# Optimization experiments

Hardware: AMD Instinct MI355X
Metric: run time of the kernel (lower is better)

The kernel has to match this reference:

```python
import math
import jax, jax.numpy as jnp
import numpy as np

NUM_HEADS = 16
LN_EPS = 1e-5


def _ln(x, g, b):
    m = x.mean(-1, keepdims=True)
    v = ((x - m) ** 2).mean(-1, keepdims=True)
    return (x - m) * jax.lax.rsqrt(v + LN_EPS) * g + b


def _rotary_embedding(lat, lon, dim, base=10000.0):
    # spherical-geometry-aware rotary phases; returns sin/cos of shape lat.shape + [dim//2]
    pi = jnp.asarray(math.pi, lat.dtype)
    lon_wrapped = jnp.remainder(lon + pi, 2 * pi) - pi
    lat_c = jnp.clip(lat, -math.pi / 2 + 1e-6, math.pi / 2 - 1e-6)
    scaled_lon = lon_wrapped * jnp.cos(lat_c)
    half = dim // 2
    inv_freq = 1.0 / (base ** (jnp.arange(half, dtype=lat.dtype) / half))
    phase = (lat_c + scaled_lon)[..., None] * inv_freq
    return jnp.sin(phase), jnp.cos(phase)


def _apply_rotary(q, k, sin, cos):
    # q,k: [N, heads, S, hd]; sin/cos: [S, hd//2]
    sin = sin[None, None]
    cos = cos[None, None]
    def rot(x):
        x1 = x[..., 0::2]  # even lanes (torch view(...,hd//2,2).unbind(-1))
        x2 = x[..., 1::2]
        # torch concatenates the two rotated halves (no re-interleave)
        return jnp.concatenate([x1 * cos - x2 * sin, x1 * sin + x2 * cos], axis=-1)
    return rot(q), rot(k)


def _sdpa(q, k, v):
    scale = 1.0 / jnp.sqrt(jnp.asarray(q.shape[-1], q.dtype))
    s = jnp.einsum('nhqd,nhkd->nhqk', q, k) * scale
    return jnp.einsum('nhqk,nhkd->nhqd', jax.nn.softmax(s, axis=-1), v)


def _axial_block(tokens, g, bln, qkv_w, qkv_b, proj_w, proj_b, sincos):
    # tokens: [N, S, D] -> norm -> qkv -> (rope) -> sdpa -> proj -> residual
    N, S, D = tokens.shape
    hd = D // NUM_HEADS
    qkv = _ln(tokens, g, bln) @ qkv_w + qkv_b
    q, k, v = jnp.split(qkv, 3, axis=-1)
    def to_heads(t):
        return t.reshape(N, S, NUM_HEADS, hd).transpose(0, 2, 1, 3)
    q, k, v = to_heads(q), to_heads(k), to_heads(v)
    if sincos is not None:
        q, k = _apply_rotary(q, k, sincos[0], sincos[1])
    o = _sdpa(q, k, v).transpose(0, 2, 1, 3).reshape(N, S, D)
    return tokens + (o @ proj_w + proj_b)


def setup_inputs() -> dict:
    key = jax.random.key(0)
    ks = jax.random.split(key, 8)
    B, L, H, W, D = 1, 13, 48, 96, 512
    x = jax.random.normal(ks[0], (B, L, H, W, D), dtype=jnp.float32)
    lat_grid = jnp.linspace(-math.pi / 2 + 0.01, math.pi / 2 - 0.01, H, dtype=jnp.float32)
    lon_grid = jnp.linspace(-math.pi, math.pi, W, dtype=jnp.float32)  # unused by forward
    s = 0.02
    return {
        'x': x, 'lat_grid': lat_grid, 'lon_grid': lon_grid,
        'lat_qkv_w': s * jax.random.normal(ks[1], (D, 3 * D), jnp.float32),
        'lat_qkv_b': jnp.zeros((3 * D,), jnp.float32),
        'lon_qkv_w': s * jax.random.normal(ks[2], (D, 3 * D), jnp.float32),
        'lon_qkv_b': jnp.zeros((3 * D,), jnp.float32),
        'lev_qkv_w': s * jax.random.normal(ks[3], (D, 3 * D), jnp.float32),
        'lev_qkv_b': jnp.zeros((3 * D,), jnp.float32),
        'proj_w': s * jax.random.normal(ks[4], (D, D), jnp.float32),
        'proj_b': jnp.zeros((D,), jnp.float32),
        'g_lat': jnp.ones((D,), jnp.float32), 'b_lat': jnp.zeros((D,), jnp.float32),
        'g_lon': jnp.ones((D,), jnp.float32), 'b_lon': jnp.zeros((D,), jnp.float32),
        'g_lev': jnp.ones((D,), jnp.float32), 'b_lev': jnp.zeros((D,), jnp.float32),
    }


def reference(x, lat_grid, lon_grid, lat_qkv_w, lat_qkv_b, lon_qkv_w, lon_qkv_b,
              lev_qkv_w, lev_qkv_b, proj_w, proj_b,
              g_lat, b_lat, g_lon, b_lon, g_lev, b_lev):
    B, L, H, W, D = x.shape
    hd = D // NUM_HEADS
    # --- lat axis ---
    lat_tokens = x.transpose(0, 1, 3, 2, 4).reshape(B * L * W, H, D)
    lat_sin, lat_cos = _rotary_embedding(lat_grid, jnp.zeros_like(lat_grid), hd)
    lat_out = _axial_block(lat_tokens, g_lat, b_lat, lat_qkv_w, lat_qkv_b,
                           proj_w, proj_b, (lat_sin, lat_cos))
    lat_out = lat_out.reshape(B, L, W, H, D).transpose(0, 1, 3, 2, 4)
    # --- lon axis ---
    lon_tokens = lat_out.reshape(B * L * H, W, D)
    lon_range = jnp.linspace(-math.pi, math.pi, W, dtype=x.dtype)
    lon_sin, lon_cos = _rotary_embedding(jnp.zeros_like(lon_range), lon_range, hd)
    lon_out = _axial_block(lon_tokens, g_lon, b_lon, lon_qkv_w, lon_qkv_b,
                           proj_w, proj_b, (lon_sin, lon_cos))
    lon_out = lon_out.reshape(B, L, H, W, D)
    # --- level axis (no rotary) ---
    lev_tokens = lon_out.transpose(0, 2, 3, 1, 4).reshape(B * H * W, L, D)
    lev_out = _axial_block(lev_tokens, g_lev, b_lev, lev_qkv_w, lev_qkv_b,
                           proj_w, proj_b, None)
    return lev_out.reshape(B, H, W, L, D).transpose(0, 3, 1, 2, 4)
```

## Files before the change

### kernel.cpp

```cpp
#include <hip/hip_runtime.h>
#include <cstdint>


#define L_DIM 13
#define H_DIM 48
#define W_DIM 96
#define D_DIM 512
#define NH    16
#define MTOK  (L_DIM * H_DIM * W_DIM)
#define N3    (3 * D_DIM)
#define PI_F  3.14159265358979323846f

typedef __bf16 bf16x8 __attribute__((ext_vector_type(8)));
typedef float  f32x4  __attribute__((ext_vector_type(4)));

__device__ __forceinline__ float bf2f(unsigned short u) {
    return __builtin_bit_cast(float, ((unsigned)u) << 16);
}
__device__ __forceinline__ unsigned short f2bf(float f) {
    unsigned u = __builtin_bit_cast(unsigned, f);
    u += 0x7fffu + ((u >> 16) & 1u);
    return (unsigned short)(u >> 16);
}
__device__ __forceinline__ void gload16(unsigned short* lds, const unsigned short* g) {
    __builtin_amdgcn_global_load_lds(
        (const __attribute__((address_space(1))) unsigned int*)g,
        (__attribute__((address_space(3))) unsigned int*)lds, 16, 0, 0);
}

__global__ __launch_bounds__(256) void transpose_w(const float* __restrict__ w,
                                                   unsigned short* __restrict__ wt, int N) {
    __shared__ unsigned short t[64][65];
    const int k0 = blockIdx.x * 64, n0 = blockIdx.y * 64;
    const int tid = threadIdx.x;
    #pragma unroll
    for (int j = 0; j < 16; ++j) {
        int lin = j * 256 + tid;
        int kr = lin >> 6, nc = lin & 63;
        t[kr][nc] = f2bf(w[(size_t)(k0 + kr) * N + n0 + nc]);
    }
    __syncthreads();
    #pragma unroll
    for (int j = 0; j < 16; ++j) {
        int lin = j * 256 + tid;
        int nr = lin >> 6, kc = lin & 63;
        wt[(size_t)(n0 + nr) * 512 + k0 + kc] = t[kc][nr];
    }
}

__global__ __launch_bounds__(256) void ln_apply(
    const float* __restrict__ src, const float* __restrict__ g,
    const float* __restrict__ bln, unsigned short* __restrict__ out)
{
    int wv = threadIdx.x >> 6, lane = threadIdx.x & 63;
    int t = blockIdx.x * 4 + wv;
    const float* p = src + (size_t)t * 512 + lane * 8;
    float4 a = *(const float4*)p, b = *(const float4*)(p + 4);
    float s  = a.x + a.y + a.z + a.w + b.x + b.y + b.z + b.w;
    float s2 = a.x*a.x + a.y*a.y + a.z*a.z + a.w*a.w + b.x*b.x + b.y*b.y + b.z*b.z + b.w*b.w;
    #pragma unroll
    for (int off = 1; off < 64; off <<= 1) {
        s  += __shfl_xor(s, off, 64);
        s2 += __shfl_xor(s2, off, 64);
    }
    float mu = s * (1.f / 512.f);
    float rs = rsqrtf(s2 * (1.f / 512.f) - mu * mu + 1e-5f);
    float4 g0 = *(const float4*)(g + lane * 8),  g1 = *(const float4*)(g + lane * 8 + 4);
    float4 b0 = *(const float4*)(bln + lane * 8), b1 = *(const float4*)(bln + lane * 8 + 4);
    unsigned short o[8];
    o[0] = f2bf((a.x - mu) * rs * g0.x + b0.x);
    o[1] = f2bf((a.y - mu) * rs * g0.y + b0.y);
    o[2] = f2bf((a.z - mu) * rs * g0.z + b0.z);
    o[3] = f2bf((a.w - mu) * rs * g0.w + b0.w);
    o[4] = f2bf((b.x - mu) * rs * g1.x + b1.x);
    o[5] = f2bf((b.y - mu) * rs * g1.y + b1.y);
    o[6] = f2bf((b.z - mu) * rs * g1.z + b1.z);
    o[7] = f2bf((b.w - mu) * rs * g1.w + b1.w);
    uint4 r;
    r.x = (unsigned)o[0] | ((unsigned)o[1] << 16);
    r.y = (unsigned)o[2] | ((unsigned)o[3] << 16);
    r.z = (unsigned)o[4] | ((unsigned)o[5] << 16);
    r.w = (unsigned)o[6] | ((unsigned)o[7] << 16);
    *(uint4*)&out[(size_t)t * 512 + lane * 8] = r;
}

#define QUAD(mi, A) do { \
    acc[mi][0] = __builtin_amdgcn_mfma_f32_16x16x32_bf16(b0, A, acc[mi][0], 0, 0, 0); \
    acc[mi][1] = __builtin_amdgcn_mfma_f32_16x16x32_bf16(b1, A, acc[mi][1], 0, 0, 0); \
    acc[mi][2] = __builtin_amdgcn_mfma_f32_16x16x32_bf16(b2, A, acc[mi][2], 0, 0, 0); \
    acc[mi][3] = __builtin_amdgcn_mfma_f32_16x16x32_bf16(b3, A, acc[mi][3], 0, 0, 0); \
} while (0)
#define RDA(AS, mi, ks) (*(const bf16x8*)&AS[wm + (mi) * 16 + lm][((((ks) * 4 + kq) ^ (lm & 7)) << 3)])
#define RDB(BS, ni, ks) (*(const bf16x8*)&BS[wn + (ni) * 16 + lm][((((ks) * 4 + kq) ^ (lm & 7)) << 3)])

#define KTILE(CAs, CBs, NAs, NBs, kn, ST, LAST) do {                               \
    bf16x8 a0, a1, a2, a3, b0, b1, b2, b3;                                         \
                                              \
    a0 = RDA(CAs,0,0); a1 = RDA(CAs,1,0); a2 = RDA(CAs,2,0); a3 = RDA(CAs,3,0);    \
    b0 = RDB(CBs,0,0); b1 = RDB(CBs,1,0); b2 = RDB(CBs,2,0); b3 = RDB(CBs,3,0);    \
    if (ST) {                                                                      \
        gload16(&NBs[wv * 32 +  0][0], bsrc + (size_t) 0 * 512 + (kn));            \
        gload16(&NBs[wv * 32 +  8][0], bsrc + (size_t) 8 * 512 + (kn));            \
        gload16(&NBs[wv * 32 + 16][0], bsrc + (size_t)16 * 512 + (kn));            \
        gload16(&NBs[wv * 32 + 24][0], bsrc + (size_t)24 * 512 + (kn));            \
    }                                                                              \
    __builtin_amdgcn_s_barrier();                                                  \
    __builtin_amdgcn_s_setprio(1);                                                 \
    QUAD(0, a0); QUAD(1, a1); QUAD(2, a2); QUAD(3, a3);                            \
    __builtin_amdgcn_s_setprio(0);                                                 \
    if (ST) asm volatile("s_waitcnt vmcnt(4)" ::: "memory");    \
    else    asm volatile("s_waitcnt vmcnt(0)" ::: "memory");       \
    __builtin_amdgcn_s_barrier();                                                  \
    __builtin_amdgcn_sched_barrier(0);                                             \
                             \
    a0 = RDA(CAs,4,0); a1 = RDA(CAs,5,0); a2 = RDA(CAs,6,0); a3 = RDA(CAs,7,0);    \
    if (ST) {                                                                      \
        gload16(&NAs[ar0 + 0][0], asrc + (kn));                                    \
        gload16(&NAs[ar0 + 8][0], asrc + (size_t)8 * LDA + (kn));                  \
    }                                                                              \
    __builtin_amdgcn_s_barrier();                                                  \
    __builtin_amdgcn_s_setprio(1);                                                 \
    QUAD(4, a0); QUAD(5, a1); QUAD(6, a2); QUAD(7, a3);                            \
    __builtin_amdgcn_s_setprio(0);                                                 \
    __builtin_amdgcn_s_barrier();                                                  \
                                             \
    a0 = RDA(CAs,0,1); a1 = RDA(CAs,1,1); a2 = RDA(CAs,2,1); a3 = RDA(CAs,3,1);    \
    b0 = RDB(CBs,0,1); b1 = RDB(CBs,1,1); b2 = RDB(CBs,2,1); b3 = RDB(CBs,3,1);    \
    if (ST) {                                                                      \
        gload16(&NAs[ar0 + 64][0], asrc + (size_t)64 * LDA + (kn));                \
        gload16(&NAs[ar0 + 72][0], asrc + (size_t)72 * LDA + (kn));                \
    }                                                                              \
    __builtin_amdgcn_s_barrier();                                                  \
    __builtin_amdgcn_s_setprio(1);                                                 \
    QUAD(0, a0); QUAD(1, a1); QUAD(2, a2); QUAD(3, a3);                            \
    __builtin_amdgcn_s_setprio(0);                                                 \
    __builtin_amdgcn_s_barrier();                                                  \
                                                             \
    a0 = RDA(CAs,4,1); a1 = RDA(CAs,5,1); a2 = RDA(CAs,6,1); a3 = RDA(CAs,7,1);    \
    __builtin_amdgcn_s_barrier();                                                  \
    __builtin_amdgcn_s_setprio(1);                                                 \
    QUAD(4, a0); QUAD(5, a1); QUAD(6, a2); QUAD(7, a3);                            \
    __builtin_amdgcn_s_setprio(0);                                                 \
    if (ST) asm volatile("s_waitcnt vmcnt(2)" ::: "memory");   \
    if (!LAST) __builtin_amdgcn_s_barrier();                                       \
    __builtin_amdgcn_sched_barrier(0);                                             \
} while (0)

template<int LDA, int NBX, bool PROJ>
__global__ __launch_bounds__(512, 2) void gemm8p(
    const unsigned short* __restrict__ A,
    const unsigned short* __restrict__ B,
    const float* __restrict__ bias,
    const float* __restrict__ resid,
    float* __restrict__ outf,
    unsigned short* __restrict__ outh)
{
    __shared__ alignas(16) unsigned short As0[256][64];
    __shared__ alignas(16) unsigned short As1[256][64];
    __shared__ alignas(16) unsigned short Bs0[256][64];
    __shared__ alignas(16) unsigned short Bs1[256][64];

    const int nwg = NBX * 234;
    const int orig = blockIdx.y * NBX + blockIdx.x;
    const int qq = nwg >> 3, rr = nwg & 7;
    const int xcd = orig & 7, idx = orig >> 3;
    const int swz = (xcd < rr ? xcd * (qq + 1) : rr * (qq + 1) + (xcd - rr) * qq) + idx;
    const int n0 = (swz % NBX) * 256;
    const int m0 = (swz / NBX) * 256;

    const int tid = threadIdx.x, lane = tid & 63, wv = tid >> 6;
    const int wm = (wv >> 2) * 128, wn = (wv & 3) * 64;
    const int lm = lane & 15, kq = lane >> 4;
    const int rblk = lane >> 3;
    const int sc = (((lane & 7) ^ rblk) << 3);

    const unsigned short* bsrc = B + (size_t)(n0 + wv * 32 + rblk) * 512 + sc;
    const int ar0 = (wv & 4) ? (128 + (wv & 3) * 16) : (wv * 16);
    const unsigned short* asrc = A + (size_t)(m0 + ar0 + rblk) * LDA + sc;

    f32x4 acc[8][4] = {};

    #pragma unroll
    for (int j = 0; j < 4; ++j)
        gload16(&Bs0[wv * 32 + j * 8][0], bsrc + (size_t)(j * 8) * 512);
    gload16(&As0[ar0 + 0][0], asrc);
    gload16(&As0[ar0 + 8][0], asrc + (size_t)8 * LDA);
    gload16(&As0[ar0 + 64][0], asrc + (size_t)64 * LDA);
    gload16(&As0[ar0 + 72][0], asrc + (size_t)72 * LDA);
    asm volatile("s_waitcnt vmcnt(2)" ::: "memory");
    __builtin_amdgcn_s_barrier();
    __builtin_amdgcn_sched_barrier(0);

    for (int kt = 0; kt < 6; kt += 2) {
        KTILE(As0, Bs0, As1, Bs1, (kt + 1) * 64, true, false);
        KTILE(As1, Bs1, As0, Bs0, (kt + 2) * 64, true, false);
    }
    KTILE(As0, Bs0, As1, Bs1, 7 * 64, true, false);
    KTILE(As1, Bs1, As0, Bs0, 0, false, true);

    const int cr = kq << 2;
    if constexpr (!PROJ) {
        #pragma unroll
        for (int ni = 0; ni < 4; ++ni) {
            const int col = n0 + wn + ni * 16 + cr;
            const float4 bb = *(const float4*)&bias[col];
            #pragma unroll
            for (int mi = 0; mi < 8; ++mi) {
                const size_t off = (size_t)(m0 + wm + mi * 16 + lm) * N3 + col;
                uint2 pk;
                pk.x = (unsigned)f2bf(acc[mi][ni][0] + bb.x) | ((unsigned)f2bf(acc[mi][ni][1] + bb.y) << 16);
                pk.y = (unsigned)f2bf(acc[mi][ni][2] + bb.z) | ((unsigned)f2bf(acc[mi][ni][3] + bb.w) << 16);
                *(uint2*)&outh[off] = pk;
            }
        }
    } else {
        #pragma unroll
        for (int ni = 0; ni < 4; ++ni) {
            const int col = n0 + wn + ni * 16 + cr;
            const float4 bb = *(const float4*)&bias[col];
            #pragma unroll
            for (int mi = 0; mi < 8; ++mi) {
                const size_t off = (size_t)(m0 + wm + mi * 16 + lm) * 512 + col;
                float4 rs = *(const float4*)&resid[off];
                float4 o;
                o.x = rs.x + acc[mi][ni][0] + bb.x;
                o.y = rs.y + acc[mi][ni][1] + bb.y;
                o.z = rs.z + acc[mi][ni][2] + bb.z;
                o.w = rs.w + acc[mi][ni][3] + bb.w;
                *(float4*)&outf[off] = o;
            }
        }
    }
}

template<int S, int MODE>
__global__ __launch_bounds__(256) void attn_big(
    unsigned short* __restrict__ qkv,
    const float* __restrict__ lat_grid, const float* __restrict__ lon_grid)
{
    constexpr int NQ  = S / 16;
    constexpr int SKP = (S + 31) & ~31;
    constexpr int VST = SKP + 8;
    __shared__ alignas(16) unsigned short qs[S][40];
    __shared__ alignas(16) unsigned short ks[S][40];
    __shared__ alignas(16) unsigned short vT[32][VST];
    __shared__ alignas(16) unsigned short pb[4][16][VST];

    const int n = blockIdx.x, h = blockIdx.y;
    const int tid = threadIdx.x, lane = tid & 63, wv = tid >> 6;
    int base, step;
    if (MODE == 0) { int l = n / 96, w = n - l * 96; base = l * 4608 + w; step = 96; }
    else           { base = n * 96; step = 1; }

    const float SCALE = 0.17677669529663689f;
    for (int idx = tid; idx < S * 16; idx += 256) {
        int s = idx >> 4, i = idx & 15;
        size_t ro = (size_t)(base + s * step) * N3 + h * 32;
        unsigned qp = *(const unsigned*)(qkv + ro + 2 * i);
        unsigned kp = *(const unsigned*)(qkv + ro + 512 + 2 * i);
        unsigned vp = *(const unsigned*)(qkv + ro + 1024 + 2 * i);
        float coord;
        if (MODE == 0) {
            float la = lat_grid[s];
            coord = fminf(fmaxf(la, -PI_F / 2 + 1e-6f), PI_F / 2 - 1e-6f);
        } else {
            float xp = lon_grid[s] + PI_F;
            coord = xp - floorf(xp * (0.5f / PI_F)) * (2.f * PI_F) - PI_F;
        }
        float ph = coord * exp2f(-(float)i * 0.83048202372f);
        float sn = sinf(ph), cs = cosf(ph);
        float q1 = bf2f((unsigned short)qp), q2 = bf2f((unsigned short)(qp >> 16));
        float k1 = bf2f((unsigned short)kp), k2 = bf2f((unsigned short)(kp >> 16));
        qs[s][i]      = f2bf((q1 * cs - q2 * sn) * SCALE);
        qs[s][16 + i] = f2bf((q1 * sn + q2 * cs) * SCALE);
        ks[s][i]      = f2bf(k1 * cs - k2 * sn);
        ks[s][16 + i] = f2bf(k1 * sn + k2 * cs);
        vT[2 * i][s]     = (unsigned short)vp;
        vT[2 * i + 1][s] = (unsigned short)(vp >> 16);
    }
    if (SKP > S) {
        for (int idx = tid; idx < 32 * (SKP - S); idx += 256)
            vT[idx / (SKP - S)][S + idx % (SKP - S)] = 0;
    }
    __syncthreads();

    const int lm = lane & 15, ko = (lane >> 4) * 8, q4 = (lane >> 4) * 4;
    f32x4 zero = {0.f, 0.f, 0.f, 0.f};
    bf16x8 vf[SKP / 32][2];
    #pragma unroll
    for (int u2 = 0; u2 < SKP / 32; ++u2)
        #pragma unroll
        for (int nh2 = 0; nh2 < 2; ++nh2)
            vf[u2][nh2] = *(const bf16x8*)&vT[nh2 * 16 + lm][u2 * 32 + ko];
    if (SKP > S) {
        for (int idx = lane; idx < 16 * (SKP - S); idx += 64)
            pb[wv][idx / (SKP - S)][S + idx % (SKP - S)] = 0;
    }

    for (int t = wv; t < NQ; t += 4) {
        bf16x8 aq = *(const bf16x8*)&qs[t * 16 + lm][ko];
        f32x4 c[NQ];
        #pragma unroll
        for (int u = 0; u < NQ; ++u) {
            bf16x8 bk = *(const bf16x8*)&ks[u * 16 + lm][ko];
            c[u] = __builtin_amdgcn_mfma_f32_16x16x32_bf16(aq, bk, zero, 0, 0, 0);
        }
        float mr[4] = {-1e30f, -1e30f, -1e30f, -1e30f}, sm[4] = {0.f, 0.f, 0.f, 0.f};
        #pragma unroll
        for (int u = 0; u < NQ; ++u)
            #pragma unroll
            for (int r = 0; r < 4; ++r) mr[r] = fmaxf(mr[r], c[u][r]);
        #pragma unroll
        for (int r = 0; r < 4; ++r)
            #pragma unroll
            for (int off = 1; off < 16; off <<= 1)
                mr[r] = fmaxf(mr[r], __shfl_xor(mr[r], off, 64));
        #pragma unroll
        for (int u = 0; u < NQ; ++u)
            #pragma unroll
            for (int r = 0; r < 4; ++r) {
                float e = __expf(c[u][r] - mr[r]);
                c[u][r] = e; sm[r] += e;
            }
        #pragma unroll
        for (int r = 0; r < 4; ++r) {
            #pragma unroll
            for (int off = 1; off < 16; off <<= 1)
                sm[r] += __shfl_xor(sm[r], off, 64);
            sm[r] = 1.f / sm[r];
        }
        #pragma unroll
        for (int u = 0; u < NQ; ++u)
            #pragma unroll
            for (int r = 0; r < 4; ++r)
                pb[wv][q4 + r][u * 16 + lm] = f2bf(c[u][r] * sm[r]);
        __builtin_amdgcn_wave_barrier();
        f32x4 o0 = zero, o1 = zero;
        #pragma unroll
        for (int u2 = 0; u2 < SKP / 32; ++u2) {
            bf16x8 ap = *(const bf16x8*)&pb[wv][lm][u2 * 32 + ko];
            o0 = __builtin_amdgcn_mfma_f32_16x16x32_bf16(ap, vf[u2][0], o0, 0, 0, 0);
            o1 = __builtin_amdgcn_mfma_f32_16x16x32_bf16(ap, vf[u2][1], o1, 0, 0, 0);
        }
        __builtin_amdgcn_wave_barrier();
        #pragma unroll
        for (int r = 0; r < 4; ++r) {
            int row = t * 16 + q4 + r;
            size_t ro = (size_t)(base + row * step) * N3 + h * 32;
            qkv[ro + lm]      = f2bf(o0[r]);
            qkv[ro + 16 + lm] = f2bf(o1[r]);
        }
    }
}

__global__ __launch_bounds__(256) void attn_small(unsigned short* __restrict__ qkv)
{
    __shared__ alignas(16) unsigned short qs[4][16][40];
    __shared__ alignas(16) unsigned short ks[4][16][40];
    __shared__ alignas(16) unsigned short vT[4][32][40];
    __shared__ alignas(16) unsigned short pb[4][16][40];
    const int tid = threadIdx.x, lane = tid & 63, wv = tid >> 6;
    const int pair = blockIdx.x * 4 + wv;
    const int n = pair >> 4, h = pair & 15;
    const int base = n, step = 4608;

    for (int idx = lane; idx < 13 * 16; idx += 64) {
        int s = idx >> 4, i = idx & 15;
        size_t ro = (size_t)(base + s * step) * N3 + h * 32;
        *(unsigned*)&qs[wv][s][2 * i] = *(const unsigned*)(qkv + ro + 2 * i);
        *(unsigned*)&ks[wv][s][2 * i] = *(const unsigned*)(qkv + ro + 512 + 2 * i);
        unsigned vp = *(const unsigned*)(qkv + ro + 1024 + 2 * i);
        vT[wv][2 * i][s]     = (unsigned short)vp;
        vT[wv][2 * i + 1][s] = (unsigned short)(vp >> 16);
    }
    for (int idx = lane; idx < 32 * 19; idx += 64) {
        int d = idx / 19, k = 13 + idx % 19;
        vT[wv][d][k] = 0;
    }
    for (int idx = lane; idx < 16 * 16; idx += 64)
        pb[wv][idx >> 4][16 + (idx & 15)] = 0;
    __syncthreads();

    const int lm = lane & 15, ko = (lane >> 4) * 8, q4 = (lane >> 4) * 4;
    f32x4 zero = {0.f, 0.f, 0.f, 0.f};
    bf16x8 aq = *(const bf16x8*)&qs[wv][lm][ko];
    bf16x8 bk = *(const bf16x8*)&ks[wv][lm][ko];
    f32x4 c = __builtin_amdgcn_mfma_f32_16x16x32_bf16(aq, bk, zero, 0, 0, 0);
    const float SCALE = 0.17677669529663689f;
    float cf[4], mr[4], sm[4];
    bool colok = (lm < 13);
    #pragma unroll
    for (int r = 0; r < 4; ++r) {
        cf[r] = colok ? c[r] * SCALE : -1e30f;
        mr[r] = cf[r];
    }
    #pragma unroll
    for (int r = 0; r < 4; ++r)
        #pragma unroll
        for (int off = 1; off < 16; off <<= 1)
            mr[r] = fmaxf(mr[r], __shfl_xor(mr[r], off, 64));
    #pragma unroll
    for (int r = 0; r < 4; ++r) { cf[r] = __expf(cf[r] - mr[r]); sm[r] = cf[r]; }
    #pragma unroll
    for (int r = 0; r < 4; ++r) {
        #pragma unroll
        for (int off = 1; off < 16; off <<= 1)
            sm[r] += __shfl_xor(sm[r], off, 64);
        sm[r] = 1.f / sm[r];
    }
    #pragma unroll
    for (int r = 0; r < 4; ++r)
        pb[wv][q4 + r][lm] = f2bf(cf[r] * sm[r]);
    __builtin_amdgcn_wave_barrier();
    bf16x8 ap  = *(const bf16x8*)&pb[wv][lm][ko];
    bf16x8 vf0 = *(const bf16x8*)&vT[wv][lm][ko];
    bf16x8 vf1 = *(const bf16x8*)&vT[wv][16 + lm][ko];
    f32x4 o0 = __builtin_amdgcn_mfma_f32_16x16x32_bf16(ap, vf0, zero, 0, 0, 0);
    f32x4 o1 = __builtin_amdgcn_mfma_f32_16x16x32_bf16(ap, vf1, zero, 0, 0, 0);
    #pragma unroll
    for (int r = 0; r < 4; ++r) {
        int row = q4 + r;
        if (row < 13) {
            size_t ro = (size_t)(base + row * step) * N3 + h * 32;
            qkv[ro + lm]      = f2bf(o0[r]);
            qkv[ro + 16 + lm] = f2bf(o1[r]);
        }
    }
}

extern "C" void kernel_launch(void* const* d_in, const int* in_sizes, int n_in,
                              void* d_out, int out_size, void* d_ws, size_t ws_size,
                              hipStream_t stream) {
    const float* x        = (const float*)d_in[0];
    const float* lat_grid = (const float*)d_in[1];
    const float* lon_grid = (const float*)d_in[2];
    const float* qkv_w[3] = {(const float*)d_in[3], (const float*)d_in[5], (const float*)d_in[7]};
    const float* qkv_b[3] = {(const float*)d_in[4], (const float*)d_in[6], (const float*)d_in[8]};
    const float* proj_w   = (const float*)d_in[9];
    const float* proj_b   = (const float*)d_in[10];
    const float* g[3]     = {(const float*)d_in[11], (const float*)d_in[13], (const float*)d_in[15]};
    const float* bln[3]   = {(const float*)d_in[12], (const float*)d_in[14], (const float*)d_in[16]};
    float* tok = (float*)d_out;

    unsigned short* wT0 = (unsigned short*)d_ws;
    unsigned short* wT1 = wT0 + 1536 * 512;
    unsigned short* wT2 = wT1 + 1536 * 512;
    unsigned short* pT  = wT2 + 1536 * 512;
    unsigned short* lnb = pT + 512 * 512;
    unsigned short* qkv = lnb + (size_t)MTOK * 512;
    unsigned short* wT[3] = {wT0, wT1, wT2};

    transpose_w<<<dim3(8, 24), 256, 0, stream>>>(qkv_w[0], wT0, 1536);
    transpose_w<<<dim3(8, 24), 256, 0, stream>>>(qkv_w[1], wT1, 1536);
    transpose_w<<<dim3(8, 24), 256, 0, stream>>>(qkv_w[2], wT2, 1536);
    transpose_w<<<dim3(8, 8),  256, 0, stream>>>(proj_w, pT, 512);

    for (int b = 0; b < 3; ++b) {
        const float* src = (b == 0) ? x : tok;
        ln_apply<<<MTOK / 4, 256, 0, stream>>>(src, g[b], bln[b], lnb);
        gemm8p<512, 6, false><<<dim3(6, MTOK / 256), 512, 0, stream>>>(
            lnb, wT[b], qkv_b[b], nullptr, nullptr, qkv);
        if (b == 0)
            attn_big<48, 0><<<dim3(L_DIM * W_DIM, NH), 256, 0, stream>>>(qkv, lat_grid, lon_grid);
        else if (b == 1)
            attn_big<96, 1><<<dim3(L_DIM * H_DIM, NH), 256, 0, stream>>>(qkv, lat_grid, lon_grid);
        else
            attn_small<<<(H_DIM * W_DIM * NH) / 4, 256, 0, stream>>>(qkv);
        gemm8p<1536, 2, true><<<dim3(2, MTOK / 256), 512, 0, stream>>>(
            qkv, pT, proj_b, src, tok, nullptr);
    }
}
```

Baseline: 1.254 ms.

## Replace ping-pong barrier schedule with single-barrier-per-tile GEMM K-loop

```diff
diff --git a/kernel.cpp b/kernel.cpp
--- a/kernel.cpp
+++ b/kernel.cpp
@@ -84,66 +84,61 @@
     *(uint4*)&out[(size_t)t * 512 + lane * 8] = r;
 }
 
-#define QUAD(mi, A) do { \
-    acc[mi][0] = __builtin_amdgcn_mfma_f32_16x16x32_bf16(b0, A, acc[mi][0], 0, 0, 0); \
-    acc[mi][1] = __builtin_amdgcn_mfma_f32_16x16x32_bf16(b1, A, acc[mi][1], 0, 0, 0); \
-    acc[mi][2] = __builtin_amdgcn_mfma_f32_16x16x32_bf16(b2, A, acc[mi][2], 0, 0, 0); \
-    acc[mi][3] = __builtin_amdgcn_mfma_f32_16x16x32_bf16(b3, A, acc[mi][3], 0, 0, 0); \
+#define MFMA4(mi, A, B0, B1, B2, B3) do { \
+    acc[mi][0] = __builtin_amdgcn_mfma_f32_16x16x32_bf16(B0, A, acc[mi][0], 0, 0, 0); \
+    acc[mi][1] = __builtin_amdgcn_mfma_f32_16x16x32_bf16(B1, A, acc[mi][1], 0, 0, 0); \
+    acc[mi][2] = __builtin_amdgcn_mfma_f32_16x16x32_bf16(B2, A, acc[mi][2], 0, 0, 0); \
+    acc[mi][3] = __builtin_amdgcn_mfma_f32_16x16x32_bf16(B3, A, acc[mi][3], 0, 0, 0); \
 } while (0)
 #define RDA(AS, mi, ks) (*(const bf16x8*)&AS[wm + (mi) * 16 + lm][((((ks) * 4 + kq) ^ (lm & 7)) << 3)])
 #define RDB(BS, ni, ks) (*(const bf16x8*)&BS[wn + (ni) * 16 + lm][((((ks) * 4 + kq) ^ (lm & 7)) << 3)])
+#define SBAR() __builtin_amdgcn_sched_barrier(0)
 
 #define KTILE(CAs, CBs, NAs, NBs, kn, ST, LAST) do {                               \
-    bf16x8 a0, a1, a2, a3, b0, b1, b2, b3;                                         \
-                                              \
-    a0 = RDA(CAs,0,0); a1 = RDA(CAs,1,0); a2 = RDA(CAs,2,0); a3 = RDA(CAs,3,0);    \
-    b0 = RDB(CBs,0,0); b1 = RDB(CBs,1,0); b2 = RDB(CBs,2,0); b3 = RDB(CBs,3,0);    \
     if (ST) {                                                                      \
         gload16(&NBs[wv * 32 +  0][0], bsrc + (size_t) 0 * 512 + (kn));            \
         gload16(&NBs[wv * 32 +  8][0], bsrc + (size_t) 8 * 512 + (kn));            \
         gload16(&NBs[wv * 32 + 16][0], bsrc + (size_t)16 * 512 + (kn));            \
         gload16(&NBs[wv * 32 + 24][0], bsrc + (size_t)24 * 512 + (kn));            \
-    }                                                                              \
-    __builtin_amdgcn_s_barrier();                                                  \
-    __builtin_amdgcn_s_setprio(1);                                                 \
-    QUAD(0, a0); QUAD(1, a1); QUAD(2, a2); QUAD(3, a3);                            \
-    __builtin_amdgcn_s_setprio(0);                                                 \
-    if (ST) asm volatile("s_waitcnt vmcnt(4)" ::: "memory");    \
-    else    asm volatile("s_waitcnt vmcnt(0)" ::: "memory");       \
-    __builtin_amdgcn_s_barrier();                                                  \
-    __builtin_amdgcn_sched_barrier(0);                                             \
-                             \
-    a0 = RDA(CAs,4,0); a1 = RDA(CAs,5,0); a2 = RDA(CAs,6,0); a3 = RDA(CAs,7,0);    \
-    if (ST) {                                                                      \
-        gload16(&NAs[ar0 + 0][0], asrc + (kn));                                    \
-        gload16(&NAs[ar0 + 8][0], asrc + (size_t)8 * LDA + (kn));                  \
-    }                                                                              \
-    __builtin_amdgcn_s_barrier();                                                  \
-    __builtin_amdgcn_s_setprio(1);                                                 \
-    QUAD(4, a0); QUAD(5, a1); QUAD(6, a2); QUAD(7, a3);                            \
-    __builtin_amdgcn_s_setprio(0);                                                 \
-    __builtin_amdgcn_s_barrier();                                                  \
-                                             \
-    a0 = RDA(CAs,0,1); a1 = RDA(CAs,1,1); a2 = RDA(CAs,2,1); a3 = RDA(CAs,3,1);    \
-    b0 = RDB(CBs,0,1); b1 = RDB(CBs,1,1); b2 = RDB(CBs,2,1); b3 = RDB(CBs,3,1);    \
-    if (ST) {                                                                      \
+        gload16(&NAs[ar0 +  0][0], asrc + (kn));                                   \
+        gload16(&NAs[ar0 +  8][0], asrc + (size_t) 8 * LDA + (kn));                \
         gload16(&NAs[ar0 + 64][0], asrc + (size_t)64 * LDA + (kn));                \
         gload16(&NAs[ar0 + 72][0], asrc + (size_t)72 * LDA + (kn));                \
     }                                                                              \
-    __builtin_amdgcn_s_barrier();                                                  \
+    SBAR();                                                                        \
+    bf16x8 xa0 = RDA(CAs,0,0), xa1 = RDA(CAs,1,0), xa2 = RDA(CAs,2,0), xa3 = RDA(CAs,3,0); \
+    bf16x8 xb0 = RDB(CBs,0,0), xb1 = RDB(CBs,1,0), xb2 = RDB(CBs,2,0), xb3 = RDB(CBs,3,0); \
+    bf16x8 ya0 = RDA(CAs,4,0), ya1 = RDA(CAs,5,0), ya2 = RDA(CAs,6,0), ya3 = RDA(CAs,7,0); \
+    SBAR();                                                                        \
     __builtin_amdgcn_s_setprio(1);                                                 \
-    QUAD(0, a0); QUAD(1, a1); QUAD(2, a2); QUAD(3, a3);                            \
+    MFMA4(0, xa0, xb0, xb1, xb2, xb3); MFMA4(1, xa1, xb0, xb1, xb2, xb3);          \
+    MFMA4(2, xa2, xb0, xb1, xb2, xb3); MFMA4(3, xa3, xb0, xb1, xb2, xb3);          \
     __builtin_amdgcn_s_setprio(0);                                                 \
-    __builtin_amdgcn_s_barrier();                                                  \
-                                                             \
-    a0 = RDA(CAs,4,1); a1 = RDA(CAs,5,1); a2 = RDA(CAs,6,1); a3 = RDA(CAs,7,1);    \
-    __builtin_amdgcn_s_barrier();                                                  \
+    SBAR();                                                                        \
+    bf16x8 za0 = RDA(CAs,0,1), za1 = RDA(CAs,1,1), za2 = RDA(CAs,2,1), za3 = RDA(CAs,3,1); \
+    bf16x8 zb0 = RDB(CBs,0,1), zb1 = RDB(CBs,1,1), zb2 = RDB(CBs,2,1), zb3 = RDB(CBs,3,1); \
+    SBAR();                                                                        \
     __builtin_amdgcn_s_setprio(1);                                                 \
-    QUAD(4, a0); QUAD(5, a1); QUAD(6, a2); QUAD(7, a3);                            \
+    MFMA4(4, ya0, xb0, xb1, xb2, xb3); MFMA4(5, ya1, xb0, xb1, xb2, xb3);          \
+    MFMA4(6, ya2, xb0, xb1, xb2, xb3); MFMA4(7, ya3, xb0, xb1, xb2, xb3);          \
     __builtin_amdgcn_s_setprio(0);                                                 \
-    if (ST) asm volatile("s_waitcnt vmcnt(2)" ::: "memory");   \
-    if (!LAST) __builtin_amdgcn_s_barrier();                                       \
-    __builtin_amdgcn_sched_barrier(0);                                             \
+    SBAR();                                                                        \
+    bf16x8 wa0 = RDA(CAs,4,1), wa1 = RDA(CAs,5,1), wa2 = RDA(CAs,6,1), wa3 = RDA(CAs,7,1); \
+    SBAR();                                                                        \
+    __builtin_amdgcn_s_setprio(1);                                                 \
+    MFMA4(0, za0, zb0, zb1, zb2, zb3); MFMA4(1, za1, zb0, zb1, zb2, zb3);          \
+    MFMA4(2, za2, zb0, zb1, zb2, zb3); MFMA4(3, za3, zb0, zb1, zb2, zb3);          \
+    __builtin_amdgcn_s_setprio(0);                                                 \
+    SBAR();                                                                        \
+    __builtin_amdgcn_s_setprio(1);                                                 \
+    MFMA4(4, wa0, zb0, zb1, zb2, zb3); MFMA4(5, wa1, zb0, zb1, zb2, zb3);          \
+    MFMA4(6, wa2, zb0, zb1, zb2, zb3); MFMA4(7, wa3, zb0, zb1, zb2, zb3);          \
+    __builtin_amdgcn_s_setprio(0);                                                 \
+    if (!LAST) {                                                                   \
+        asm volatile("s_waitcnt vmcnt(0)" ::: "memory");                           \
+        __builtin_amdgcn_s_barrier();                                              \
+        SBAR();                                                                    \
+    }                                                                              \
 } while (0)
 
 template<int LDA, int NBX, bool PROJ>
@@ -180,14 +175,15 @@
 
     f32x4 acc[8][4] = {};
 
-    #pragma unroll
-    for (int j = 0; j < 4; ++j)
-        gload16(&Bs0[wv * 32 + j * 8][0], bsrc + (size_t)(j * 8) * 512);
-    gload16(&As0[ar0 + 0][0], asrc);
-    gload16(&As0[ar0 + 8][0], asrc + (size_t)8 * LDA);
+    gload16(&Bs0[wv * 32 +  0][0], bsrc + (size_t) 0 * 512);
+    gload16(&Bs0[wv * 32 +  8][0], bsrc + (size_t) 8 * 512);
+    gload16(&Bs0[wv * 32 + 16][0], bsrc + (size_t)16 * 512);
+    gload16(&Bs0[wv * 32 + 24][0], bsrc + (size_t)24 * 512);
+    gload16(&As0[ar0 +  0][0], asrc);
+    gload16(&As0[ar0 +  8][0], asrc + (size_t) 8 * LDA);
     gload16(&As0[ar0 + 64][0], asrc + (size_t)64 * LDA);
     gload16(&As0[ar0 + 72][0], asrc + (size_t)72 * LDA);
-    asm volatile("s_waitcnt vmcnt(2)" ::: "memory");
+    asm volatile("s_waitcnt vmcnt(0)" ::: "memory");
     __builtin_amdgcn_s_barrier();
     __builtin_amdgcn_sched_barrier(0);
 
```

Result: no change. 1.236 ms (-1.4%).
